# Kernel optimization log

Hardware: AMD Instinct MI355X
Metric: run time of the kernel (lower is better)

Reference implementation:

```python
import jax, jax.numpy as jnp
import numpy as np

TOP_K = 4


def setup_inputs() -> dict:
    key = jax.random.key(0)
    ks = jax.random.split(key, 6)
    B, S, H, I, E = 2, 1024, 1024, 1024, 16
    SD = I * 1  # shared_dim = moe_intermediate_size * n_shared_experts
    s = 0.02
    return {
        "hidden_states": jax.random.normal(ks[0], (B, S, H), jnp.float32),
        "gate_w": jax.random.normal(ks[1], (E, H), jnp.float32) * s,
        "w1": jax.random.normal(ks[2], (E, I, H), jnp.float32) * s,
        "w2": jax.random.normal(ks[3], (E, H, I), jnp.float32) * s,
        "shared_gu": jax.random.normal(ks[4], (2 * SD, H), jnp.float32) * s,
        "shared_down": jax.random.normal(ks[5], (H, SD), jnp.float32) * s,
    }


def reference(hidden_states, gate_w, w1, w2, shared_gu, shared_down):
    orig_shape = hidden_states.shape
    H = orig_shape[-1]
    x = hidden_states.reshape(-1, H)            # [T, H]
    T = x.shape[0]
    E = gate_w.shape[0]

    # --- router: softmax -> top-k -> renormalize ---
    logits = x @ gate_w.T                       # [T, E]
    probs = jax.nn.softmax(logits, axis=-1)
    topv, topi = jax.lax.top_k(probs, TOP_K)    # [T, K]
    topv = topv / jnp.sum(topv, axis=-1, keepdims=True)
    # dense routing-weight matrix [T, E] (zero for unselected experts)
    W = jnp.zeros((T, E), x.dtype).at[jnp.arange(T)[:, None], topi].set(topv)

    # --- routed experts: silu(x @ w1[e].T) @ w2[e].T, weighted ---
    h = jax.nn.silu(jnp.einsum('th,eih->tei', x, w1))      # [T, E, I]
    routed = jnp.einsum('tei,ehi,te->th', h, w2, W)        # [T, H]

    # --- shared expert SwiGLU ---
    gu = x @ shared_gu.T                        # [T, 2*SD]
    gate, up = jnp.split(gu, 2, axis=-1)
    shared = (jax.nn.silu(gate) * up) @ shared_down.T      # [T, H]

    return (routed + shared).reshape(orig_shape)
```

## Files before the change

kernel.cpp:

```cpp
#include <hip/hip_runtime.h>
#include <hip/hip_bf16.h>
#include <math.h>

using bf16 = __hip_bfloat16;

typedef __attribute__((ext_vector_type(4))) float fv4;
typedef __attribute__((ext_vector_type(4))) short sh4;
typedef __attribute__((ext_vector_type(8))) short sh8;
typedef __attribute__((ext_vector_type(4))) float f4acc;

#define T_TOK 2048
#define HD    1024
#define NE    16
#define KD    1024
#define NPAIR 8192

static constexpr size_t OFF_XB    = 0;
static constexpr size_t OFF_GUB   = 4194304;
static constexpr size_t OFF_ACT   = 12582912;
static constexpr size_t OFF_H1    = 16777216;
static constexpr size_t OFF_W2B   = 33554432;
static constexpr size_t OFF_SDNB  = 67108864;
static constexpr size_t OFF_TOPI  = 69206016;
static constexpr size_t OFF_TOPV  = 69238784;
static constexpr size_t OFF_PTOK  = 69271552;
static constexpr size_t OFF_PWT   = 69304320;
static constexpr size_t OFF_OFFS  = 69337088;
static constexpr size_t OFF_CNT   = 69337600;
static constexpr size_t OFF_CBASE = 69338112;

__device__ __forceinline__ short f2bf(float f) {
  __hip_bfloat16 h = __float2bfloat16(f);
  union { __hip_bfloat16 b; short s; } u; u.b = h; return u.s;
}
__device__ __forceinline__ float bf2f(short s) {
  union { unsigned u; float f; } c; c.u = ((unsigned)(unsigned short)s) << 16; return c.f;
}
__device__ __forceinline__ void async16(const void* g, void* l) {
  __builtin_amdgcn_global_load_lds(
      (const __attribute__((address_space(1))) void*)g,
      (__attribute__((address_space(3))) void*)l, 16, 0, 0);
}

__global__ __launch_bounds__(256) void router_kernel(const float* __restrict__ x,
                                                     const float* __restrict__ gw,
                                                     int* __restrict__ topi,
                                                     float* __restrict__ topv,
                                                     short* __restrict__ xb,
                                                     float* __restrict__ out) {
  __shared__ float gsh[NE * HD];
  const int tid = threadIdx.x;
  const int wave = tid >> 6;
  const int lane = tid & 63;
  const int t = blockIdx.x * 4 + wave;

#pragma unroll
  for (int r = 0; r < 16; ++r) {
    int idx = r * 256 + tid;
    ((fv4*)gsh)[idx] = ((const fv4*)gw)[idx];
  }

  const float* xr = x + (size_t)t * HD;
  fv4 xa[4];
#pragma unroll
  for (int q = 0; q < 4; ++q) xa[q] = *(const fv4*)(xr + q * 256 + lane * 4);

#pragma unroll
  for (int q = 0; q < 4; ++q) {
    sh4 o; o[0]=f2bf(xa[q][0]); o[1]=f2bf(xa[q][1]); o[2]=f2bf(xa[q][2]); o[3]=f2bf(xa[q][3]);
    *(sh4*)(xb + (size_t)t * HD + q * 256 + lane * 4) = o;
    *(fv4*)(out + (size_t)t * HD + q * 256 + lane * 4) = (fv4)(0.f);
  }

  __syncthreads();

  float p[NE];
#pragma unroll
  for (int e = 0; e < NE; ++e) {
    const float* g = gsh + e * HD;
    float a = 0.f;
#pragma unroll
    for (int q = 0; q < 4; ++q) {
      fv4 gv = *(const fv4*)(g + q * 256 + lane * 4);
      a += xa[q][0] * gv[0] + xa[q][1] * gv[1] + xa[q][2] * gv[2] + xa[q][3] * gv[3];
    }
    p[e] = a;
  }
#pragma unroll
  for (int off = 1; off < 64; off <<= 1) {
#pragma unroll
    for (int e = 0; e < NE; ++e) p[e] += __shfl_xor(p[e], off);
  }

  int sel_i[4]; float sel_v[4];
#pragma unroll
  for (int k = 0; k < 4; ++k) {
    float best = p[0]; int bi = 0;
#pragma unroll
    for (int e = 1; e < NE; ++e) {
      bool c = p[e] > best;
      best = c ? p[e] : best;
      bi   = c ? e : bi;
    }
    sel_i[k] = bi; sel_v[k] = best;
#pragma unroll
    for (int e = 0; e < NE; ++e) p[e] = (e == bi) ? -3.4e38f : p[e];
  }
  float m = sel_v[0];
  float e0 = expf(sel_v[0] - m), e1 = expf(sel_v[1] - m);
  float e2 = expf(sel_v[2] - m), e3 = expf(sel_v[3] - m);
  float inv = 1.f / (e0 + e1 + e2 + e3);

  if (lane == 0) {
    topi[t * 4 + 0] = sel_i[0]; topv[t * 4 + 0] = e0 * inv;
    topi[t * 4 + 1] = sel_i[1]; topv[t * 4 + 1] = e1 * inv;
    topi[t * 4 + 2] = sel_i[2]; topv[t * 4 + 2] = e2 * inv;
    topi[t * 4 + 3] = sel_i[3]; topv[t * 4 + 3] = e3 * inv;
  }
}

__global__ __launch_bounds__(1024) void count_kernel(const int* __restrict__ topi,
                                                     int* __restrict__ cnt) {
  const int b = blockIdx.x;
  const int wave = threadIdx.x >> 6;
  const int lane = threadIdx.x & 63;
  const int base = b * 1024;
  int c = 0;
#pragma unroll
  for (int i = 0; i < 16; ++i) {
    unsigned long long m = __ballot(topi[base + i * 64 + lane] == wave);
    c += __popcll(m);
  }
  if (lane == 0) cnt[b * NE + wave] = c;
}

__global__ void scan2_kernel(const int* __restrict__ cnt,
                             int* __restrict__ offsets,
                             int* __restrict__ cbase) {
  if (threadIdx.x == 0 && blockIdx.x == 0) {
    int acc = 0;
    for (int e = 0; e < NE; ++e) {
      offsets[e] = acc;
      for (int b = 0; b < 8; ++b) { cbase[b * NE + e] = acc; acc += cnt[b * NE + e]; }
    }
    offsets[NE] = acc;
  }
}

__global__ __launch_bounds__(1024) void compact_kernel(const int* __restrict__ topi,
                                                       const float* __restrict__ topv,
                                                       const int* __restrict__ cbase,
                                                       int* __restrict__ ptok,
                                                       float* __restrict__ pwt) {
  const int b = blockIdx.x;
  const int wave = threadIdx.x >> 6;
  const int lane = threadIdx.x & 63;
  const int base = b * 1024;
  int slot = cbase[b * NE + wave];
#pragma unroll
  for (int i = 0; i < 16; ++i) {
    const int p = base + i * 64 + lane;
    const bool match = (topi[p] == wave);
    unsigned long long m = __ballot(match);
    unsigned long long lt = (lane == 0) ? 0ull : ((~0ull) >> (64 - lane));
    int pre = __popcll(m & lt);
    if (match) { ptok[slot + pre] = p >> 2; pwt[slot + pre] = topv[p]; }
    slot += __popcll(m);
  }
}

__global__ __launch_bounds__(256) void act_kernel(const short* __restrict__ gub,
                                                  short* __restrict__ act) {
  int i = blockIdx.x * 256 + threadIdx.x;
  int t = i >> 8, g = i & 255;
  sh4 gs = *(const sh4*)(gub + (size_t)t * 2048 + g * 4);
  sh4 us = *(const sh4*)(gub + (size_t)t * 2048 + 1024 + g * 4);
  sh4 o;
#pragma unroll
  for (int q = 0; q < 4; ++q) {
    float gg = bf2f(gs[q]);
    float s = gg / (1.f + expf(-gg)) * bf2f(us[q]);
    o[q] = f2bf(s);
  }
  *(sh4*)(act + (size_t)t * 1024 + g * 4) = o;
}

__global__ __launch_bounds__(256) void gemm_k2_kernel(
    const bf16* __restrict__ A_sh, const bf16* __restrict__ A_rt,
    const float* __restrict__ B_sh, const float* __restrict__ B_rt,
    const float* __restrict__ w2, const float* __restrict__ sdn,
    short* __restrict__ w2b, short* __restrict__ sdnb,
    void* __restrict__ O_sh, void* __restrict__ O_rt,
    const int* __restrict__ ptok, const float* __restrict__ pwt,
    const int* __restrict__ offsets) {
  __shared__ bf16 Ash[2][128][32];
  __shared__ bf16 Bsh[2][128][32];

  const int tid = threadIdx.x;
  const int lane = tid & 63;
  const int wave = tid >> 6;
  const int wm = wave >> 1, wn = wave & 1;

  if ((int)blockIdx.x < 2048) {
    const size_t base = (size_t)blockIdx.x * 2048 + tid;
#pragma unroll
    for (int it = 0; it < 8; ++it) {
      fv4 v = ((const fv4*)w2)[base + it * 256];
      sh4 o; o[0]=f2bf(v[0]); o[1]=f2bf(v[1]); o[2]=f2bf(v[2]); o[3]=f2bf(v[3]);
      ((sh4*)w2b)[base + it * 256] = o;
    }
  } else {
    const size_t base = (size_t)(blockIdx.x - 2048) * 1024 + tid;
#pragma unroll
    for (int it = 0; it < 4; ++it) {
      fv4 v = ((const fv4*)sdn)[base + it * 256];
      sh4 o; o[0]=f2bf(v[0]); o[1]=f2bf(v[1]); o[2]=f2bf(v[2]); o[3]=f2bf(v[3]);
      ((sh4*)sdnb)[base + it * 256] = o;
    }
  }

  const bool routed = (int)blockIdx.x < 2048;
  int mt, nt, seg_start = 0, count = 0;
  const bf16* Abase;
  const float* Bpanel;
  if (routed) {
    int bid = blockIdx.x;
    int e = bid & 15;
    int r = bid >> 4;
    mt = r >> 3; nt = r & 7;
    seg_start = offsets[e];
    count = offsets[e + 1] - seg_start;
    if (mt * 128 >= count) return;
    Abase = A_rt;
    Bpanel = B_rt + ((size_t)e << 20) + (size_t)(nt * 128) * KD;
  } else {
    int sb = blockIdx.x - 2048;
    constexpr int cpx = 256 >> 3;
    int sw = (sb & 7) * cpx + (sb >> 3);
    nt = sw >> 4; mt = sw & 15;
    count = 1 << 30;
    Abase = A_sh;
    Bpanel = B_sh + (size_t)(nt * 128) * KD;
  }

  const bf16* arow[2];
#pragma unroll
  for (int r = 0; r < 2; ++r) {
    int rowloc = r * 64 + wave * 16 + (lane >> 2);
    int grow;
    if (routed) {
      int slot = seg_start + mt * 128 + rowloc;
      if (slot > NPAIR - 1) slot = NPAIR - 1;
      grow = ptok[slot];
    } else {
      grow = mt * 128 + rowloc;
    }
    arow[r] = Abase + (size_t)grow * KD + (lane & 3) * 8;
  }

  const float* brow[4];
  int bwrow[4], bwcol[4];
#pragma unroll
  for (int r = 0; r < 4; ++r) {
    int idx = (r << 8) + tid;
    int row = idx >> 3, cg = idx & 7;
    brow[r] = Bpanel + (size_t)row * KD + (cg << 2);
    bwrow[r] = row; bwcol[r] = cg << 2;
  }

  f4acc acc[4][4];
#pragma unroll
  for (int i = 0; i < 4; ++i)
#pragma unroll
    for (int j = 0; j < 4; ++j) acc[i][j] = (f4acc)(0.f);

  {
    fv4 b0 = *(const fv4*)(brow[0]);
    fv4 b1 = *(const fv4*)(brow[1]);
    fv4 b2 = *(const fv4*)(brow[2]);
    fv4 b3 = *(const fv4*)(brow[3]);
    async16(arow[0], (void*)&Ash[0][wave * 16][0]);
    async16(arow[1], (void*)&Ash[0][64 + wave * 16][0]);
    sh4 p0; p0[0]=f2bf(b0[0]); p0[1]=f2bf(b0[1]); p0[2]=f2bf(b0[2]); p0[3]=f2bf(b0[3]);
    sh4 p1; p1[0]=f2bf(b1[0]); p1[1]=f2bf(b1[1]); p1[2]=f2bf(b1[2]); p1[3]=f2bf(b1[3]);
    sh4 p2; p2[0]=f2bf(b2[0]); p2[1]=f2bf(b2[1]); p2[2]=f2bf(b2[2]); p2[3]=f2bf(b2[3]);
    sh4 p3; p3[0]=f2bf(b3[0]); p3[1]=f2bf(b3[1]); p3[2]=f2bf(b3[2]); p3[3]=f2bf(b3[3]);
    *(sh4*)&Bsh[0][bwrow[0]][bwcol[0]] = p0;
    *(sh4*)&Bsh[0][bwrow[1]][bwcol[1]] = p1;
    *(sh4*)&Bsh[0][bwrow[2]][bwcol[2]] = p2;
    *(sh4*)&Bsh[0][bwrow[3]][bwcol[3]] = p3;
  }
  __syncthreads();

  int buf = 0;
  for (int kt = 0; kt < 32; ++kt) {
    const int k0n = (kt + 1) * 32;
    const bool has_next = (kt < 31);
    fv4 n0, n1, n2, n3;
    if (has_next) {
      async16(arow[0] + k0n, (void*)&Ash[buf ^ 1][wave * 16][0]);
      async16(arow[1] + k0n, (void*)&Ash[buf ^ 1][64 + wave * 16][0]);
      n0 = *(const fv4*)(brow[0] + k0n);
      n1 = *(const fv4*)(brow[1] + k0n);
      n2 = *(const fv4*)(brow[2] + k0n);
      n3 = *(const fv4*)(brow[3] + k0n);
    }

    sh8 fa[4], fb[4];
#pragma unroll
    for (int mi = 0; mi < 4; ++mi)
      fa[mi] = *(const sh8*)&Ash[buf][wm * 64 + mi * 16 + (lane & 15)][(lane >> 4) * 8];
#pragma unroll
    for (int ni = 0; ni < 4; ++ni)
      fb[ni] = *(const sh8*)&Bsh[buf][wn * 64 + ni * 16 + (lane & 15)][(lane >> 4) * 8];
#pragma unroll
    for (int mi = 0; mi < 4; ++mi)
#pragma unroll
      for (int ni = 0; ni < 4; ++ni)
        acc[mi][ni] = __builtin_amdgcn_mfma_f32_16x16x32_bf16(fa[mi], fb[ni], acc[mi][ni], 0, 0, 0);

    if (has_next) {
      sh4 p0; p0[0]=f2bf(n0[0]); p0[1]=f2bf(n0[1]); p0[2]=f2bf(n0[2]); p0[3]=f2bf(n0[3]);
      sh4 p1; p1[0]=f2bf(n1[0]); p1[1]=f2bf(n1[1]); p1[2]=f2bf(n1[2]); p1[3]=f2bf(n1[3]);
      sh4 p2; p2[0]=f2bf(n2[0]); p2[1]=f2bf(n2[1]); p2[2]=f2bf(n2[2]); p2[3]=f2bf(n2[3]);
      sh4 p3; p3[0]=f2bf(n3[0]); p3[1]=f2bf(n3[1]); p3[2]=f2bf(n3[2]); p3[3]=f2bf(n3[3]);
      *(sh4*)&Bsh[buf ^ 1][bwrow[0]][bwcol[0]] = p0;
      *(sh4*)&Bsh[buf ^ 1][bwrow[1]][bwcol[1]] = p1;
      *(sh4*)&Bsh[buf ^ 1][bwrow[2]][bwcol[2]] = p2;
      *(sh4*)&Bsh[buf ^ 1][bwrow[3]][bwcol[3]] = p3;
    }
    __syncthreads();
    buf ^= 1;
  }

  if (routed) {
#pragma unroll
    for (int mi = 0; mi < 4; ++mi) {
#pragma unroll
      for (int j = 0; j < 4; ++j) {
        int rloc = wm * 64 + mi * 16 + (lane >> 4) * 4 + j;
        if (mt * 128 + rloc >= count) continue;
        size_t orow = (size_t)(seg_start + mt * 128 + rloc) * 1024 + nt * 128;
#pragma unroll
        for (int ni = 0; ni < 4; ++ni) {
          int cloc = wn * 64 + ni * 16 + (lane & 15);
          float v = acc[mi][ni][j];
          float s = v / (1.f + expf(-v));
          ((short*)O_rt)[orow + cloc] = f2bf(s);
        }
      }
    }
  } else {
#pragma unroll
    for (int mi = 0; mi < 4; ++mi) {
#pragma unroll
      for (int j = 0; j < 4; ++j) {
        int rloc = wm * 64 + mi * 16 + (lane >> 4) * 4 + j;
        size_t orow = (size_t)(mt * 128 + rloc) * 2048 + nt * 128;
#pragma unroll
        for (int ni = 0; ni < 4; ++ni) {
          int cloc = wn * 64 + ni * 16 + (lane & 15);
          ((short*)O_sh)[orow + cloc] = f2bf(acc[mi][ni][j]);
        }
      }
    }
  }
}

__global__ __launch_bounds__(256) void gemm_k3_kernel(
    const bf16* __restrict__ A_sh, const bf16* __restrict__ A_rt,
    const bf16* __restrict__ B_sh, const bf16* __restrict__ B_rt,
    float* __restrict__ out,
    const int* __restrict__ ptok, const float* __restrict__ pwt,
    const int* __restrict__ offsets) {
  __shared__ bf16 Ash[2][128][32];
  __shared__ bf16 Bsh[2][128][32];

  const int tid = threadIdx.x;
  const int lane = tid & 63;
  const int wave = tid >> 6;
  const int wm = wave >> 1, wn = wave & 1;

  const bool routed = (int)blockIdx.x < 2048;
  int mt, nt, seg_start = 0, count = 0;
  const bf16* Abase;
  const bf16* Bpanel;
  if (routed) {
    int bid = blockIdx.x;
    int e = bid & 15;
    int r = bid >> 4;
    mt = r >> 3; nt = r & 7;
    seg_start = offsets[e];
    count = offsets[e + 1] - seg_start;
    if (mt * 128 >= count) return;
    Abase = A_rt;
    Bpanel = B_rt + ((size_t)e << 20) + (size_t)(nt * 128) * KD;
  } else {
    int sb = blockIdx.x - 2048;
    constexpr int cpx = 128 >> 3;
    int sw = (sb & 7) * cpx + (sb >> 3);
    nt = sw >> 4; mt = sw & 15;
    count = 1 << 30;
    Abase = A_sh;
    Bpanel = B_sh + (size_t)(nt * 128) * KD;
  }

  const bf16* arow[2];
  const bf16* brow[2];
#pragma unroll
  for (int r = 0; r < 2; ++r) {
    int rowloc = r * 64 + wave * 16 + (lane >> 2);
    int grow;
    if (routed) {
      int slot = seg_start + mt * 128 + rowloc;
      if (slot > NPAIR - 1) slot = NPAIR - 1;
      grow = slot;
    } else {
      grow = mt * 128 + rowloc;
    }
    arow[r] = Abase + (size_t)grow * KD + (lane & 3) * 8;
    brow[r] = Bpanel + (size_t)rowloc * KD + (lane & 3) * 8;
  }

  f4acc acc[4][4];
#pragma unroll
  for (int i = 0; i < 4; ++i)
#pragma unroll
    for (int j = 0; j < 4; ++j) acc[i][j] = (f4acc)(0.f);

  async16(arow[0], (void*)&Ash[0][wave * 16][0]);
  async16(arow[1], (void*)&Ash[0][64 + wave * 16][0]);
  async16(brow[0], (void*)&Bsh[0][wave * 16][0]);
  async16(brow[1], (void*)&Bsh[0][64 + wave * 16][0]);
  __syncthreads();

  int buf = 0;
  for (int kt = 0; kt < 32; ++kt) {
    const int k0n = (kt + 1) * 32;
    if (kt < 31) {
      async16(arow[0] + k0n, (void*)&Ash[buf ^ 1][wave * 16][0]);
      async16(arow[1] + k0n, (void*)&Ash[buf ^ 1][64 + wave * 16][0]);
      async16(brow[0] + k0n, (void*)&Bsh[buf ^ 1][wave * 16][0]);
      async16(brow[1] + k0n, (void*)&Bsh[buf ^ 1][64 + wave * 16][0]);
    }

    sh8 fa[4], fb[4];
#pragma unroll
    for (int mi = 0; mi < 4; ++mi)
      fa[mi] = *(const sh8*)&Ash[buf][wm * 64 + mi * 16 + (lane & 15)][(lane >> 4) * 8];
#pragma unroll
    for (int ni = 0; ni < 4; ++ni)
      fb[ni] = *(const sh8*)&Bsh[buf][wn * 64 + ni * 16 + (lane & 15)][(lane >> 4) * 8];
#pragma unroll
    for (int mi = 0; mi < 4; ++mi)
#pragma unroll
      for (int ni = 0; ni < 4; ++ni)
        acc[mi][ni] = __builtin_amdgcn_mfma_f32_16x16x32_bf16(fa[mi], fb[ni], acc[mi][ni], 0, 0, 0);

    __syncthreads();
    buf ^= 1;
  }

  if (routed) {
#pragma unroll
    for (int mi = 0; mi < 4; ++mi) {
#pragma unroll
      for (int j = 0; j < 4; ++j) {
        int rloc = wm * 64 + mi * 16 + (lane >> 4) * 4 + j;
        if (mt * 128 + rloc >= count) continue;
        int slot = seg_start + mt * 128 + rloc;
        int token = ptok[slot];
        float w = pwt[slot];
        float* orow = out + (size_t)token * 1024 + nt * 128;
#pragma unroll
        for (int ni = 0; ni < 4; ++ni) {
          int cloc = wn * 64 + ni * 16 + (lane & 15);
          unsafeAtomicAdd(orow + cloc, w * acc[mi][ni][j]);
        }
      }
    }
  } else {
#pragma unroll
    for (int mi = 0; mi < 4; ++mi) {
#pragma unroll
      for (int j = 0; j < 4; ++j) {
        int rloc = wm * 64 + mi * 16 + (lane >> 4) * 4 + j;
        float* orow = out + (size_t)(mt * 128 + rloc) * 1024 + nt * 128;
#pragma unroll
        for (int ni = 0; ni < 4; ++ni) {
          int cloc = wn * 64 + ni * 16 + (lane & 15);
          unsafeAtomicAdd(orow + cloc, acc[mi][ni][j]);
        }
      }
    }
  }
}

extern "C" void kernel_launch(void* const* d_in, const int* in_sizes, int n_in,
                              void* d_out, int out_size, void* d_ws, size_t ws_size,
                              hipStream_t stream) {
  const float* x   = (const float*)d_in[0];
  const float* gw  = (const float*)d_in[1];
  const float* w1  = (const float*)d_in[2];
  const float* w2  = (const float*)d_in[3];
  const float* sgu = (const float*)d_in[4];
  const float* sdn = (const float*)d_in[5];
  float* out = (float*)d_out;

  char* ws = (char*)d_ws;
  bf16*  xb    = (bf16*)(ws + OFF_XB);
  bf16*  gub   = (bf16*)(ws + OFF_GUB);
  bf16*  act   = (bf16*)(ws + OFF_ACT);
  bf16*  h1    = (bf16*)(ws + OFF_H1);
  bf16*  w2b   = (bf16*)(ws + OFF_W2B);
  bf16*  sdnb  = (bf16*)(ws + OFF_SDNB);
  int*   topi  = (int*)(ws + OFF_TOPI);
  float* topv  = (float*)(ws + OFF_TOPV);
  int*   ptok  = (int*)(ws + OFF_PTOK);
  float* pwt   = (float*)(ws + OFF_PWT);
  int*   offs  = (int*)(ws + OFF_OFFS);
  int*   cnt   = (int*)(ws + OFF_CNT);
  int*   cbase = (int*)(ws + OFF_CBASE);

  router_kernel<<<512, 256, 0, stream>>>(x, gw, topi, topv, (short*)xb, out);
  count_kernel<<<8, 1024, 0, stream>>>(topi, cnt);
  scan2_kernel<<<1, 64, 0, stream>>>(cnt, offs, cbase);
  compact_kernel<<<8, 1024, 0, stream>>>(topi, topv, cbase, ptok, pwt);

  gemm_k2_kernel<<<2304, 256, 0, stream>>>(xb, xb, sgu, w1, w2, sdn,
                                           (short*)w2b, (short*)sdnb,
                                           gub, h1, ptok, pwt, offs);
  act_kernel<<<2048, 256, 0, stream>>>((const short*)gub, (short*)act);

  gemm_k3_kernel<<<2176, 256, 0, stream>>>(act, h1, sdnb, w2b,
                                           out, ptok, pwt, offs);
}
```

Measured before the change: 165.9 us.

## Pre-cast w1 and shared gate-up to bf16 and async-load B in GEMM

Adds a cast kernel that converts w1 and shared_gu to bf16 before the first GEMM. The first GEMM can then load its B tiles with global_load_lds, the same async path already used for A, instead of fp32 register loads followed by in-loop conversion and LDS stores. The w2 and shared_down casts move out of the GEMM into a combined kernel with the SwiGLU activation, and w2's bf16 copy reuses the now-dead w1b buffer. This trades an extra full read/write pass over w1 for a lighter, fully asynchronous GEMM main loop with fewer registers.

```diff
diff --git a/kernel.cpp b/kernel.cpp
--- a/kernel.cpp
+++ b/kernel.cpp
@@ -19,15 +19,16 @@
 static constexpr size_t OFF_GUB   = 4194304;
 static constexpr size_t OFF_ACT   = 12582912;
 static constexpr size_t OFF_H1    = 16777216;
-static constexpr size_t OFF_W2B   = 33554432;
-static constexpr size_t OFF_SDNB  = 67108864;
-static constexpr size_t OFF_TOPI  = 69206016;
-static constexpr size_t OFF_TOPV  = 69238784;
-static constexpr size_t OFF_PTOK  = 69271552;
-static constexpr size_t OFF_PWT   = 69304320;
-static constexpr size_t OFF_OFFS  = 69337088;
-static constexpr size_t OFF_CNT   = 69337600;
-static constexpr size_t OFF_CBASE = 69338112;
+static constexpr size_t OFF_W1B   = 33554432;
+static constexpr size_t OFF_SGUB  = 67108864;
+static constexpr size_t OFF_SDNB  = 71303168;
+static constexpr size_t OFF_TOPI  = 73400320;
+static constexpr size_t OFF_TOPV  = 73433088;
+static constexpr size_t OFF_PTOK  = 73465856;
+static constexpr size_t OFF_PWT   = 73498624;
+static constexpr size_t OFF_OFFS  = 73531392;
+static constexpr size_t OFF_CNT   = 73531904;
+static constexpr size_t OFF_CBASE = 73532416;
 
 __device__ __forceinline__ short f2bf(float f) {
   __hip_bfloat16 h = __float2bfloat16(f);
@@ -169,28 +170,53 @@
   }
 }
 
-__global__ __launch_bounds__(256) void act_kernel(const short* __restrict__ gub,
-                                                  short* __restrict__ act) {
-  int i = blockIdx.x * 256 + threadIdx.x;
-  int t = i >> 8, g = i & 255;
-  sh4 gs = *(const sh4*)(gub + (size_t)t * 2048 + g * 4);
-  sh4 us = *(const sh4*)(gub + (size_t)t * 2048 + 1024 + g * 4);
-  sh4 o;
-#pragma unroll
-  for (int q = 0; q < 4; ++q) {
-    float gg = bf2f(gs[q]);
-    float s = gg / (1.f + expf(-gg)) * bf2f(us[q]);
-    o[q] = f2bf(s);
-  }
-  *(sh4*)(act + (size_t)t * 1024 + g * 4) = o;
+__global__ __launch_bounds__(256) void cast1_kernel(const float* __restrict__ w1,
+                                                    const float* __restrict__ sgu,
+                                                    short* __restrict__ w1b,
+                                                    short* __restrict__ sgub) {
+  int bid = blockIdx.x;
+  const float* src; short* dst; int idx;
+  if (bid < 16384) { src = w1;  dst = w1b;  idx = bid * 256 + threadIdx.x; }
+  else             { src = sgu; dst = sgub; idx = (bid - 16384) * 256 + threadIdx.x; }
+  fv4 v = ((const fv4*)src)[idx];
+  sh4 o; o[0]=f2bf(v[0]); o[1]=f2bf(v[1]); o[2]=f2bf(v[2]); o[3]=f2bf(v[3]);
+  ((sh4*)dst)[idx] = o;
+}
+
+__global__ __launch_bounds__(256) void act_w2_kernel(const float* __restrict__ w2,
+                                                     const float* __restrict__ sdn,
+                                                     short* __restrict__ w2b,
+                                                     short* __restrict__ sdnb,
+                                                     const short* __restrict__ gub,
+                                                     short* __restrict__ act) {
+  int bid = blockIdx.x;
+  if (bid < 17408) {
+    const float* src; short* dst; int idx;
+    if (bid < 16384) { src = w2;  dst = w2b;  idx = bid * 256 + threadIdx.x; }
+    else             { src = sdn; dst = sdnb; idx = (bid - 16384) * 256 + threadIdx.x; }
+    fv4 v = ((const fv4*)src)[idx];
+    sh4 o; o[0]=f2bf(v[0]); o[1]=f2bf(v[1]); o[2]=f2bf(v[2]); o[3]=f2bf(v[3]);
+    ((sh4*)dst)[idx] = o;
+  } else {
+    int i = (bid - 17408) * 256 + threadIdx.x;
+    int t = i >> 8, g = i & 255;
+    sh4 gs = *(const sh4*)(gub + (size_t)t * 2048 + g * 4);
+    sh4 us = *(const sh4*)(gub + (size_t)t * 2048 + 1024 + g * 4);
+    sh4 o;
+#pragma unroll
+    for (int q = 0; q < 4; ++q) {
+      float gg = bf2f(gs[q]);
+      float s = gg / (1.f + expf(-gg)) * bf2f(us[q]);
+      o[q] = f2bf(s);
+    }
+    *(sh4*)(act + (size_t)t * 1024 + g * 4) = o;
+  }
 }
 
 __global__ __launch_bounds__(256) void gemm_k2_kernel(
     const bf16* __restrict__ A_sh, const bf16* __restrict__ A_rt,
-    const float* __restrict__ B_sh, const float* __restrict__ B_rt,
-    const float* __restrict__ w2, const float* __restrict__ sdn,
-    short* __restrict__ w2b, short* __restrict__ sdnb,
-    void* __restrict__ O_sh, void* __restrict__ O_rt,
+    const bf16* __restrict__ B_sh, const bf16* __restrict__ B_rt,
+    short* __restrict__ O_sh, short* __restrict__ O_rt,
     const int* __restrict__ ptok, const float* __restrict__ pwt,
     const int* __restrict__ offsets) {
   __shared__ bf16 Ash[2][128][32];
@@ -201,28 +227,10 @@
   const int wave = tid >> 6;
   const int wm = wave >> 1, wn = wave & 1;
 
-  if ((int)blockIdx.x < 2048) {
-    const size_t base = (size_t)blockIdx.x * 2048 + tid;
-#pragma unroll
-    for (int it = 0; it < 8; ++it) {
-      fv4 v = ((const fv4*)w2)[base + it * 256];
-      sh4 o; o[0]=f2bf(v[0]); o[1]=f2bf(v[1]); o[2]=f2bf(v[2]); o[3]=f2bf(v[3]);
-      ((sh4*)w2b)[base + it * 256] = o;
-    }
-  } else {
-    const size_t base = (size_t)(blockIdx.x - 2048) * 1024 + tid;
-#pragma unroll
-    for (int it = 0; it < 4; ++it) {
-      fv4 v = ((const fv4*)sdn)[base + it * 256];
-      sh4 o; o[0]=f2bf(v[0]); o[1]=f2bf(v[1]); o[2]=f2bf(v[2]); o[3]=f2bf(v[3]);
-      ((sh4*)sdnb)[base + it * 256] = o;
-    }
-  }
-
   const bool routed = (int)blockIdx.x < 2048;
   int mt, nt, seg_start = 0, count = 0;
   const bf16* Abase;
-  const float* Bpanel;
+  const bf16* Bpanel;
   if (routed) {
     int bid = blockIdx.x;
     int e = bid & 15;
@@ -244,6 +252,7 @@
   }
 
   const bf16* arow[2];
+  const bf16* brow[2];
 #pragma unroll
   for (int r = 0; r < 2; ++r) {
     int rowloc = r * 64 + wave * 16 + (lane >> 2);
@@ -256,16 +265,7 @@
       grow = mt * 128 + rowloc;
     }
     arow[r] = Abase + (size_t)grow * KD + (lane & 3) * 8;
-  }
-
-  const float* brow[4];
-  int bwrow[4], bwcol[4];
-#pragma unroll
-  for (int r = 0; r < 4; ++r) {
-    int idx = (r << 8) + tid;
-    int row = idx >> 3, cg = idx & 7;
-    brow[r] = Bpanel + (size_t)row * KD + (cg << 2);
-    bwrow[r] = row; bwcol[r] = cg << 2;
+    brow[r] = Bpanel + (size_t)rowloc * KD + (lane & 3) * 8;
   }
 
   f4acc acc[4][4];
@@ -274,36 +274,20 @@
 #pragma unroll
     for (int j = 0; j < 4; ++j) acc[i][j] = (f4acc)(0.f);
 
-  {
-    fv4 b0 = *(const fv4*)(brow[0]);
-    fv4 b1 = *(const fv4*)(brow[1]);
-    fv4 b2 = *(const fv4*)(brow[2]);
-    fv4 b3 = *(const fv4*)(brow[3]);
-    async16(arow[0], (void*)&Ash[0][wave * 16][0]);
-    async16(arow[1], (void*)&Ash[0][64 + wave * 16][0]);
-    sh4 p0; p0[0]=f2bf(b0[0]); p0[1]=f2bf(b0[1]); p0[2]=f2bf(b0[2]); p0[3]=f2bf(b0[3]);
-    sh4 p1; p1[0]=f2bf(b1[0]); p1[1]=f2bf(b1[1]); p1[2]=f2bf(b1[2]); p1[3]=f2bf(b1[3]);
-    sh4 p2; p2[0]=f2bf(b2[0]); p2[1]=f2bf(b2[1]); p2[2]=f2bf(b2[2]); p2[3]=f2bf(b2[3]);
-    sh4 p3; p3[0]=f2bf(b3[0]); p3[1]=f2bf(b3[1]); p3[2]=f2bf(b3[2]); p3[3]=f2bf(b3[3]);
-    *(sh4*)&Bsh[0][bwrow[0]][bwcol[0]] = p0;
-    *(sh4*)&Bsh[0][bwrow[1]][bwcol[1]] = p1;
-    *(sh4*)&Bsh[0][bwrow[2]][bwcol[2]] = p2;
-    *(sh4*)&Bsh[0][bwrow[3]][bwcol[3]] = p3;
-  }
+  async16(arow[0], (void*)&Ash[0][wave * 16][0]);
+  async16(arow[1], (void*)&Ash[0][64 + wave * 16][0]);
+  async16(brow[0], (void*)&Bsh[0][wave * 16][0]);
+  async16(brow[1], (void*)&Bsh[0][64 + wave * 16][0]);
   __syncthreads();
 
   int buf = 0;
   for (int kt = 0; kt < 32; ++kt) {
     const int k0n = (kt + 1) * 32;
-    const bool has_next = (kt < 31);
-    fv4 n0, n1, n2, n3;
-    if (has_next) {
+    if (kt < 31) {
       async16(arow[0] + k0n, (void*)&Ash[buf ^ 1][wave * 16][0]);
       async16(arow[1] + k0n, (void*)&Ash[buf ^ 1][64 + wave * 16][0]);
-      n0 = *(const fv4*)(brow[0] + k0n);
-      n1 = *(const fv4*)(brow[1] + k0n);
-      n2 = *(const fv4*)(brow[2] + k0n);
-      n3 = *(const fv4*)(brow[3] + k0n);
+      async16(brow[0] + k0n, (void*)&Bsh[buf ^ 1][wave * 16][0]);
+      async16(brow[1] + k0n, (void*)&Bsh[buf ^ 1][64 + wave * 16][0]);
     }
 
     sh8 fa[4], fb[4];
@@ -319,16 +303,6 @@
       for (int ni = 0; ni < 4; ++ni)
         acc[mi][ni] = __builtin_amdgcn_mfma_f32_16x16x32_bf16(fa[mi], fb[ni], acc[mi][ni], 0, 0, 0);
 
-    if (has_next) {
-      sh4 p0; p0[0]=f2bf(n0[0]); p0[1]=f2bf(n0[1]); p0[2]=f2bf(n0[2]); p0[3]=f2bf(n0[3]);
-      sh4 p1; p1[0]=f2bf(n1[0]); p1[1]=f2bf(n1[1]); p1[2]=f2bf(n1[2]); p1[3]=f2bf(n1[3]);
-      sh4 p2; p2[0]=f2bf(n2[0]); p2[1]=f2bf(n2[1]); p2[2]=f2bf(n2[2]); p2[3]=f2bf(n2[3]);
-      sh4 p3; p3[0]=f2bf(n3[0]); p3[1]=f2bf(n3[1]); p3[2]=f2bf(n3[2]); p3[3]=f2bf(n3[3]);
-      *(sh4*)&Bsh[buf ^ 1][bwrow[0]][bwcol[0]] = p0;
-      *(sh4*)&Bsh[buf ^ 1][bwrow[1]][bwcol[1]] = p1;
-      *(sh4*)&Bsh[buf ^ 1][bwrow[2]][bwcol[2]] = p2;
-      *(sh4*)&Bsh[buf ^ 1][bwrow[3]][bwcol[3]] = p3;
-    }
     __syncthreads();
     buf ^= 1;
   }
@@ -346,7 +320,7 @@
           int cloc = wn * 64 + ni * 16 + (lane & 15);
           float v = acc[mi][ni][j];
           float s = v / (1.f + expf(-v));
-          ((short*)O_rt)[orow + cloc] = f2bf(s);
+          O_rt[orow + cloc] = f2bf(s);
         }
       }
     }
@@ -360,7 +334,7 @@
 #pragma unroll
         for (int ni = 0; ni < 4; ++ni) {
           int cloc = wn * 64 + ni * 16 + (lane & 15);
-          ((short*)O_sh)[orow + cloc] = f2bf(acc[mi][ni][j]);
+          O_sh[orow + cloc] = f2bf(acc[mi][ni][j]);
         }
       }
     }
@@ -512,7 +486,8 @@
   bf16*  gub   = (bf16*)(ws + OFF_GUB);
   bf16*  act   = (bf16*)(ws + OFF_ACT);
   bf16*  h1    = (bf16*)(ws + OFF_H1);
-  bf16*  w2b   = (bf16*)(ws + OFF_W2B);
+  bf16*  w1b   = (bf16*)(ws + OFF_W1B);
+  bf16*  sgub  = (bf16*)(ws + OFF_SGUB);
   bf16*  sdnb  = (bf16*)(ws + OFF_SDNB);
   int*   topi  = (int*)(ws + OFF_TOPI);
   float* topv  = (float*)(ws + OFF_TOPV);
@@ -527,11 +502,14 @@
   scan2_kernel<<<1, 64, 0, stream>>>(cnt, offs, cbase);
   compact_kernel<<<8, 1024, 0, stream>>>(topi, topv, cbase, ptok, pwt);
 
-  gemm_k2_kernel<<<2304, 256, 0, stream>>>(xb, xb, sgu, w1, w2, sdn,
-                                           (short*)w2b, (short*)sdnb,
-                                           gub, h1, ptok, pwt, offs);
-  act_kernel<<<2048, 256, 0, stream>>>((const short*)gub, (short*)act);
-
-  gemm_k3_kernel<<<2176, 256, 0, stream>>>(act, h1, sdnb, w2b,
+  cast1_kernel<<<18432, 256, 0, stream>>>(w1, sgu, (short*)w1b, (short*)sgub);
+
+  gemm_k2_kernel<<<2304, 256, 0, stream>>>(xb, xb, sgub, w1b,
+                                           (short*)gub, (short*)h1, ptok, pwt, offs);
+
+  act_w2_kernel<<<19456, 256, 0, stream>>>(w2, sdn, (short*)w1b, (short*)sdnb,
+                                           (const short*)gub, (short*)act);
+
+  gemm_k3_kernel<<<2176, 256, 0, stream>>>(act, h1, sdnb, w1b ,
                                            out, ptok, pwt, offs);
 }
```

New measurement: 180.5 us. 1.09x slower.
